# Kernel tuning notes

Hardware: AMD Instinct MI355X
Metric: run time of the kernel (lower is better)

## Reference

```python
import jax, jax.numpy as jnp
import numpy as np

NH, NOPE, ROPE, VD, KVL = 16, 128, 64, 128, 512
QHD = NOPE + ROPE  # 192
EPS = 1e-6
THETA = 10000.0


def rmsnorm(x, w):
    v = jnp.mean(x.astype(jnp.float32) ** 2, axis=-1, keepdims=True)
    return w * (x * jax.lax.rsqrt(v + EPS)).astype(x.dtype)


def _interleave_perm(x):
    # x.view(..., d//2, 2).transpose(-1, -2).reshape(..., d): [x0,x2,...,x1,x3,...]
    return jnp.concatenate([x[..., 0::2], x[..., 1::2]], axis=-1)


def _rotate_half(x):
    d = x.shape[-1] // 2
    return jnp.concatenate([-x[..., d:], x[..., :d]], axis=-1)


def _rope(x, cos, sin):
    x = _interleave_perm(x)
    return x * cos + _rotate_half(x) * sin


def reference(hidden_states, position_ids, q_a_w, q_a_ln, q_b_w, kv_a_w, kv_a_ln, kv_b_w, o_w):
    B, S, _ = hidden_states.shape
    h = hidden_states

    # low-rank Q: q_b(rmsnorm(q_a(h)))
    q = rmsnorm(h @ q_a_w.T, q_a_ln) @ q_b_w.T          # [B,S,NH*192]
    q = q.reshape(B, S, NH, QHD).transpose(0, 2, 1, 3)   # [B,NH,S,192]
    q_nope, q_pe = q[..., :NOPE], q[..., NOPE:]

    # compressed KV + shared rope key
    ckv = h @ kv_a_w.T                                    # [B,S,KVL+ROPE]
    compressed, k_pe = ckv[..., :KVL], ckv[..., KVL:]
    k_pe = k_pe.reshape(B, S, 1, ROPE).transpose(0, 2, 1, 3)  # [B,1,S,ROPE]

    kv = rmsnorm(compressed, kv_a_ln) @ kv_b_w.T          # [B,S,NH*(NOPE+VD)]
    kv = kv.reshape(B, S, NH, NOPE + VD).transpose(0, 2, 1, 3)
    k_nope, v = kv[..., :NOPE], kv[..., NOPE:]            # [B,NH,S,*]

    # rotary cache
    inv_freq = 1.0 / (THETA ** (jnp.arange(0, ROPE, 2, dtype=jnp.float32) / ROPE))
    t = jnp.arange(S, dtype=jnp.float32)
    freqs = jnp.outer(t, inv_freq)
    emb = jnp.concatenate([freqs, freqs], axis=-1)        # [S,ROPE]
    cos = jnp.cos(emb)[position_ids][:, None]             # [B,1,S,ROPE]
    sin = jnp.sin(emb)[position_ids][:, None]

    q_pe = _rope(q_pe, cos, sin)
    k_pe = _rope(k_pe, cos, sin)

    query = jnp.concatenate([q_nope, q_pe], axis=-1)                       # [B,NH,S,192]
    key = jnp.concatenate([k_nope, jnp.broadcast_to(k_pe, (B, NH, S, ROPE))], axis=-1)

    scale = QHD ** -0.5
    scores = jnp.einsum('bhqd,bhkd->bhqk', query, key) * scale
    causal = jnp.tril(jnp.ones((S, S), dtype=bool))
    scores = jnp.where(causal, scores, jnp.finfo(scores.dtype).min)
    attn = jax.nn.softmax(scores.astype(jnp.float32), axis=-1).astype(query.dtype)

    out = jnp.einsum('bhqk,bhkd->bhqd', attn, v)          # [B,NH,S,VD]
    out = out.transpose(0, 2, 1, 3).reshape(B, S, NH * VD)
    return out @ o_w.T


def setup_inputs():
    key = jax.random.key(0)
    ks = jax.random.split(key, 7)
    B, S, HID, QL = 2, 1024, 2048, 1536
    w = lambda i, shape: jax.random.normal(ks[i], shape, jnp.float32) / np.sqrt(shape[-1])
    return {
        'hidden_states': jax.random.normal(ks[0], (B, S, HID), jnp.float32),
        'position_ids': jnp.tile(jnp.arange(S, dtype=jnp.int32)[None, :], (B, 1)),
        'q_a_w': w(1, (QL, HID)),
        'q_a_ln': jnp.ones((QL,), jnp.float32),
        'q_b_w': w(2, (NH * QHD, QL)),
        'kv_a_w': w(3, (KVL + ROPE, HID)),
        'kv_a_ln': jnp.ones((KVL,), jnp.float32),
        'kv_b_w': w(4, (NH * (NOPE + VD), KVL)),
        'o_w': w(5, (HID, NH * VD)),
    }
```

## Files before the change

kernel.cpp:

```cpp
#include <hip/hip_runtime.h>
#include <stdint.h>
#include <math.h>

typedef unsigned short u16;
typedef __attribute__((ext_vector_type(8))) short short8;
typedef __attribute__((ext_vector_type(4))) short short4v;
typedef __attribute__((ext_vector_type(4))) float f32x4;

#define DEVFN static __device__ __forceinline__

DEVFN float bf2f(short b) {
  union { unsigned int i; float f; } u;
  u.i = ((unsigned int)(unsigned short)b) << 16;
  return u.f;
}
DEVFN short f2bf(float f) {
  union { float f; unsigned int i; } u; u.f = f;
  unsigned int r = u.i + 0x7fffu + ((u.i >> 16) & 1u);
  return (short)(r >> 16);
}

DEVFN f32x4 mfma32(short8 a, short8 b, f32x4 c) {
  return __builtin_amdgcn_mfma_f32_16x16x32_bf16(a, b, c, 0, 0, 0);
}
DEVFN f32x4 mfma16(short4v a, short4v b, f32x4 c) {
#if defined(__HIP_DEVICE_COMPILE__)
  return __builtin_amdgcn_mfma_f32_16x16x16bf16_1k(a, b, c, 0, 0, 0);
#else
  (void)a; (void)b; return c;
#endif
}

typedef const __attribute__((address_space(1))) unsigned int* gp_t;
typedef __attribute__((address_space(3))) unsigned int* lp_t;
typedef const __attribute__((address_space(3))) u16* lds_cp;
DEVFN void async_copy16(u16* lds, const u16* g) {
  __builtin_amdgcn_global_load_lds((gp_t)(const void*)g, (lp_t)(void*)lds, 16, 0, 0);
}
DEVFN short4v tr_read16(const u16* p) {
  short4v r;
  asm volatile("ds_read_b64_tr_b16 %0, %1" : "=v"(r) : "v"((lds_cp)(const void*)p));
  return r;
}
DEVFN void raw_barrier() {
  asm volatile("" ::: "memory");
  __builtin_amdgcn_s_barrier();
  asm volatile("" ::: "memory");
}

__global__ void cast_kernel(const float* __restrict__ in, u16* __restrict__ out, int n4) {
  int i = blockIdx.x * blockDim.x + threadIdx.x;
  if (i < n4) {
    f32x4 v = ((const f32x4*)in)[i];
    short4v o;
    o[0] = f2bf(v[0]); o[1] = f2bf(v[1]); o[2] = f2bf(v[2]); o[3] = f2bf(v[3]);
    ((short4v*)out)[i] = o;
  }
}

__global__ void rmsnorm_kernel(const u16* __restrict__ in, int istride,
                               u16* __restrict__ out, int ostride,
                               const float* __restrict__ w, int len) {
  const int row = blockIdx.x, t = threadIdx.x;
  short8 v = *(const short8*)(in + (size_t)row * istride + t * 8);
  float f[8]; float ss = 0.f;
#pragma unroll
  for (int j = 0; j < 8; ++j) { f[j] = bf2f(v[j]); ss += f[j] * f[j]; }
#pragma unroll
  for (int off = 1; off < 64; off <<= 1) ss += __shfl_xor(ss, off);
  __shared__ float red[8];
  int nw = (int)blockDim.x >> 6;
  if ((t & 63) == 0) red[t >> 6] = ss;
  __syncthreads();
  ss = 0.f;
  for (int i = 0; i < nw; ++i) ss += red[i];
  float r = rsqrtf(ss / (float)len + 1e-6f);
  const float* wp = w + t * 8;
  short8 ov;
#pragma unroll
  for (int j = 0; j < 8; ++j) ov[j] = f2bf(f[j] * r * wp[j]);
  *(short8*)(out + (size_t)row * ostride + t * 8) = ov;
}

__global__ void rope_kernel(const u16* __restrict__ q, const u16* __restrict__ ckv,
                            int cstride,
                            const int* __restrict__ pos_ids,
                            u16* __restrict__ qpe, u16* __restrict__ kpe) {
  const int row = blockIdx.x;
  const int t = threadIdx.x;
  const float pos = (float)pos_ids[row];
  const float L2TH = 13.287712379549449f;
  if (t < 32) {
    int i = t;
    float inv = exp2f(-L2TH * (float)i / 32.0f);
    float sv, cv; sincosf(pos * inv, &sv, &cv);
    float x0 = bf2f(ckv[(size_t)row * cstride + 512 + 2 * i]);
    float x1 = bf2f(ckv[(size_t)row * cstride + 512 + 2 * i + 1]);
    kpe[(size_t)row * 64 + i]      = (u16)f2bf(x0 * cv - x1 * sv);
    kpe[(size_t)row * 64 + 32 + i] = (u16)f2bf(x1 * cv + x0 * sv);
  }
#pragma unroll
  for (int j = 0; j < 8; ++j) {
    int idx = t + 64 * j;
    int hh = idx >> 5, i = idx & 31;
    float inv = exp2f(-L2TH * (float)i / 32.0f);
    float sv, cv; sincosf(pos * inv, &sv, &cv);
    const u16* base = q + (size_t)row * 3072 + hh * 192 + 128;
    float x0 = bf2f(base[2 * i]), x1 = bf2f(base[2 * i + 1]);
    u16* ob = qpe + ((size_t)row * 16 + hh) * 64;
    ob[i]      = (u16)f2bf(x0 * cv - x1 * sv);
    ob[32 + i] = (u16)f2bf(x1 * cv + x0 * sv);
  }
}

template <int BM, int BN, bool OUT_F32, int TAG>
__global__ __launch_bounds__(256) void gemm_bt(const u16* __restrict__ A,
                                               const u16* __restrict__ B,
                                               void* __restrict__ C,
                                               int M, int N, int K, int ldc) {
  constexpr int ACH = BM / 32;
  constexpr int BCH = BN / 32;
  constexpr int MI  = BM / 32;
  constexpr int NI  = BN / 32;
  constexpr int LOADS = ACH + BCH;
  __shared__ u16 As[2][BM * 64];
  __shared__ u16 Bs[2][BN * 64];
  const int tid = threadIdx.x;
  const int w = tid >> 6, l = tid & 63;
  const int lq = l & 15, lg = l >> 4;
  const int wm = (w >> 1) * (BM / 2);
  const int wn = (w & 1) * (BN / 2);

  const int f = blockIdx.x + gridDim.x * blockIdx.y;
  const int nwg = gridDim.x * gridDim.y;
  const int swz = (f & 7) * (nwg >> 3) + (f >> 3);
  const int bx = swz % gridDim.x, by = swz / gridDim.x;
  const int m0 = by * BM, n0 = bx * BN;

  const u16* srcA[ACH]; int dstA[ACH];
#pragma unroll
  for (int i = 0; i < ACH; ++i) {
    int c = i * 256 + tid;
    int row = c >> 3, pc = c & 7;
    int lc = pc ^ (row & 7);
    srcA[i] = A + (size_t)(m0 + row) * K + lc * 8;
    dstA[i] = c * 8;
  }
  const u16* srcB[BCH]; int dstB[BCH];
#pragma unroll
  for (int i = 0; i < BCH; ++i) {
    int c = i * 256 + tid;
    int row = c >> 3, pc = c & 7;
    int lc = pc ^ (row & 7);
    srcB[i] = B + (size_t)(n0 + row) * K + lc * 8;
    dstB[i] = c * 8;
  }

  auto stage = [&](int buf) {
#pragma unroll
    for (int i = 0; i < ACH; ++i) {
      async_copy16(&As[buf][dstA[i]], srcA[i]);
      srcA[i] += 64;
    }
#pragma unroll
    for (int i = 0; i < BCH; ++i) {
      async_copy16(&Bs[buf][dstB[i]], srcB[i]);
      srcB[i] += 64;
    }
  };

  f32x4 acc[MI][NI];
#pragma unroll
  for (int i = 0; i < MI; ++i)
#pragma unroll
    for (int j = 0; j < NI; ++j) acc[i][j] = (f32x4){0.f, 0.f, 0.f, 0.f};

  const int nt = K >> 6;
  stage(0);
  if (nt > 1) stage(1);

  for (int t = 0; t < nt; ++t) {
    if (t + 1 < nt) {
      if constexpr (LOADS == 4)      asm volatile("s_waitcnt vmcnt(4)" ::: "memory");
      else if constexpr (LOADS == 6) asm volatile("s_waitcnt vmcnt(6)" ::: "memory");
      else                           asm volatile("s_waitcnt vmcnt(8)" ::: "memory");
    } else {
      asm volatile("s_waitcnt vmcnt(0)" ::: "memory");
    }
    raw_barrier();

    const int buf = t & 1;
#pragma unroll
    for (int ks = 0; ks < 2; ++ks) {
      short8 af[MI], bfr[NI];
#pragma unroll
      for (int mi = 0; mi < MI; ++mi) {
        int row = wm + mi * 16 + lq;
        int ch = ((ks << 2) | lg) ^ (row & 7);
        af[mi] = *(const short8*)&As[buf][row * 64 + ch * 8];
      }
#pragma unroll
      for (int ni = 0; ni < NI; ++ni) {
        int row = wn + ni * 16 + lq;
        int ch = ((ks << 2) | lg) ^ (row & 7);
        bfr[ni] = *(const short8*)&Bs[buf][row * 64 + ch * 8];
      }
#pragma unroll
      for (int mi = 0; mi < MI; ++mi)
#pragma unroll
        for (int ni = 0; ni < NI; ++ni)
          acc[mi][ni] = mfma32(af[mi], bfr[ni], acc[mi][ni]);
    }

    raw_barrier();
    if (t + 2 < nt) stage(buf);
  }

#pragma unroll
  for (int mi = 0; mi < MI; ++mi) {
#pragma unroll
    for (int ni = 0; ni < NI; ++ni) {
      int col = n0 + wn + ni * 16 + lq;
#pragma unroll
      for (int r = 0; r < 4; ++r) {
        int rowm = m0 + wm + mi * 16 + lg * 4 + r;
        if constexpr (OUT_F32)
          ((float*)C)[(size_t)rowm * ldc + col] = acc[mi][ni][r];
        else
          ((u16*)C)[(size_t)rowm * ldc + col] = (u16)f2bf(acc[mi][ni][r]);
      }
    }
  }
}

__global__ __launch_bounds__(512, 4) void attn_kernel(const u16* __restrict__ q,
                                                      const u16* __restrict__ qpe,
                                                      const u16* __restrict__ kv,
                                                      const u16* __restrict__ kpe,
                                                      u16* __restrict__ o) {
  __shared__ u16 Ks[2][2][32 * 192];
  __shared__ u16 Vs[2][2][32 * 128];
  const int S = 1024;
  const int tid = threadIdx.x;
  const int w = tid >> 6, l = tid & 63;
  const int team = w >> 2, wt = w & 3;
  const int lq = l & 15, lg = l >> 4;
  const int h = blockIdx.y, b = blockIdx.z;
  const int chunk = b ? (15 - (int)blockIdx.x) : (int)blockIdx.x;
  const int q0 = chunk * 64 + wt * 16;
  const int nkt = chunk + 1;
  const size_t qrow = (size_t)b * S + q0 + lq;

  short8 qf[6];
#pragma unroll
  for (int c = 0; c < 4; ++c)
    qf[c] = *(const short8*)(q + qrow * 3072 + h * 192 + c * 32 + lg * 8);
#pragma unroll
  for (int c = 0; c < 2; ++c)
    qf[4 + c] = *(const short8*)(qpe + (qrow * 16 + h) * 64 + c * 32 + lg * 8);

  const size_t gb = (size_t)b * S + 32 * team;
  const u16* srcK[3]; int strK[3];
#pragma unroll
  for (int j = 0; j < 3; ++j) {
    int n = wt * 192 + j * 64 + l;
    int row = (n * 2731) >> 16;
    int pc = n - row * 24;
    int lc = (pc & ~7) | ((pc & 7) ^ (row & 7));
    if (lc < 16) { srcK[j] = kv + (gb + row) * 4096 + h * 256 + lc * 8; strK[j] = 64 * 4096; }
    else         { srcK[j] = kpe + (gb + row) * 64 + (lc - 16) * 8;     strK[j] = 64 * 64; }
  }
  const u16* srcV[2];
#pragma unroll
  for (int j = 0; j < 2; ++j) {
    int n = wt * 128 + j * 64 + l;
    int dsub = n >> 6, m = n & 63;
    int ksub = m >> 3, r = (m >> 1) & 3, half = m & 1;
    srcV[j] = kv + (gb + ksub * 4 + r) * 4096 + h * 256 + 128 + dsub * 16 + half * 8;
  }

  auto stage = [&](int buf) {
#pragma unroll
    for (int j = 0; j < 3; ++j) {
      async_copy16(&Ks[buf][team][(wt * 192 + j * 64) * 8], srcK[j]);
      srcK[j] += strK[j];
    }
#pragma unroll
    for (int j = 0; j < 2; ++j) {
      async_copy16(&Vs[buf][team][(wt * 128 + j * 64) * 8], srcV[j]);
      srcV[j] += 64 * 4096;
    }
  };

  const float scl = 0.07216878364870323f * 1.4426950408889634f;
  float m2 = -INFINITY, lsum = 0.f;
  f32x4 oac[8];
#pragma unroll
  for (int dt = 0; dt < 8; ++dt) oac[dt] = (f32x4){0.f, 0.f, 0.f, 0.f};

  const int e0 = (lg ^ (lq & 7)) << 4;
  const int vbase = lg * 64 + lq * 4;

  stage(0);
  asm volatile("s_waitcnt vmcnt(0)" ::: "memory");
  __syncthreads();

  int buf = 0;
  for (int i = 0; i < nkt; ++i) {
    if (i + 1 < nkt) stage(buf ^ 1);
    const int kbase = (2 * i + team) * 32;

    if (kbase <= q0 + 15) {
      const char* kb = (const char*)&Ks[buf][team][0];
      f32x4 sac0, sac1;
#pragma unroll
      for (int kt2 = 0; kt2 < 2; ++kt2) {
        int a0 = (kt2 * 16 + lq) * 384 + e0;
        int a1 = a0 ^ 64;
        f32x4 s = (f32x4){0.f, 0.f, 0.f, 0.f};
        s = mfma32(*(const short8*)(kb + a0),       qf[0], s);
        s = mfma32(*(const short8*)(kb + a1),       qf[1], s);
        s = mfma32(*(const short8*)(kb + a0 + 128), qf[2], s);
        s = mfma32(*(const short8*)(kb + a1 + 128), qf[3], s);
        s = mfma32(*(const short8*)(kb + a0 + 256), qf[4], s);
        s = mfma32(*(const short8*)(kb + a1 + 256), qf[5], s);
        if (kt2 == 0) sac0 = s; else sac1 = s;
      }

      const int qi = q0 + lq;
      const int kb0 = kbase + lg * 4;
      float s2[8];
#pragma unroll
      for (int r = 0; r < 4; ++r) {
        s2[r]     = (kb0 + r      <= qi) ? sac0[r] * scl : -INFINITY;
        s2[4 + r] = (kb0 + 16 + r <= qi) ? sac1[r] * scl : -INFINITY;
      }
      float mt = fmaxf(fmaxf(fmaxf(s2[0], s2[1]), fmaxf(s2[2], s2[3])),
                       fmaxf(fmaxf(s2[4], s2[5]), fmaxf(s2[6], s2[7])));
      mt = fmaxf(mt, __shfl_xor(mt, 16));
      mt = fmaxf(mt, __shfl_xor(mt, 32));
      float mnew = fmaxf(m2, mt);
      float resc = exp2f(m2 - mnew);
      float psum = 0.f;
#pragma unroll
      for (int r = 0; r < 8; ++r) { s2[r] = exp2f(s2[r] - mnew); psum += s2[r]; }
      psum += __shfl_xor(psum, 16);
      psum += __shfl_xor(psum, 32);
      lsum = lsum * resc + psum;
      m2 = mnew;
      short4v pf0, pf1;
#pragma unroll
      for (int r = 0; r < 4; ++r) { pf0[r] = f2bf(s2[r]); pf1[r] = f2bf(s2[4 + r]); }

#pragma unroll
      for (int hf = 0; hf < 2; ++hf) {
        short4v vf[4][2];
#pragma unroll
        for (int dd = 0; dd < 4; ++dd)
#pragma unroll
          for (int kt2 = 0; kt2 < 2; ++kt2)
            vf[dd][kt2] = tr_read16(&Vs[buf][team][vbase + (hf * 4 + dd) * 512 + kt2 * 256]);
        asm volatile("s_waitcnt lgkmcnt(0)" ::: "memory");
        __builtin_amdgcn_sched_barrier(0);
#pragma unroll
        for (int dd = 0; dd < 4; ++dd) {
          const int dt = hf * 4 + dd;
          f32x4 t = oac[dt];
          t[0] *= resc; t[1] *= resc; t[2] *= resc; t[3] *= resc;
          t = mfma16(vf[dd][0], pf0, t);
          t = mfma16(vf[dd][1], pf1, t);
          oac[dt] = t;
        }
      }
    }

    asm volatile("s_waitcnt vmcnt(0)" ::: "memory");
    __syncthreads();
    buf ^= 1;
  }

  float* MO = (float*)&Ks[0][0][0];
  float* MS = (float*)&Vs[0][0][0];
  const int qr = wt * 16 + lq;
  if (team == 1) {
#pragma unroll
    for (int dt = 0; dt < 8; ++dt)
#pragma unroll
      for (int r = 0; r < 4; ++r)
        MO[qr * 129 + dt * 16 + lg * 4 + r] = oac[dt][r];
    if (lg == 0) { MS[qr * 2] = m2; MS[qr * 2 + 1] = lsum; }
  }
  __syncthreads();
  if (team == 0) {
    float m1 = MS[qr * 2], l1 = MS[qr * 2 + 1];
    float mn = fmaxf(m2, m1);
    float a0 = exp2f(m2 - mn), a1 = exp2f(m1 - mn);
    float inv = 1.f / (lsum * a0 + l1 * a1);
#pragma unroll
    for (int dt = 0; dt < 8; ++dt)
#pragma unroll
      for (int r = 0; r < 4; ++r) {
        float val = (oac[dt][r] * a0 + MO[qr * 129 + dt * 16 + lg * 4 + r] * a1) * inv;
        o[((size_t)b * S + q0 + lq) * 2048 + h * 128 + dt * 16 + lg * 4 + r] = (u16)f2bf(val);
      }
  }
}

extern "C" void kernel_launch(void* const* d_in, const int* in_sizes, int n_in,
                              void* d_out, int out_size, void* d_ws, size_t ws_size,
                              hipStream_t stream) {
  const float* h_in  = (const float*)d_in[0];
  const int*   pos   = (const int*)d_in[1];
  const float* qaw   = (const float*)d_in[2];
  const float* qaln  = (const float*)d_in[3];
  const float* qbw   = (const float*)d_in[4];
  const float* kvaw  = (const float*)d_in[5];
  const float* kvaln = (const float*)d_in[6];
  const float* kvbw  = (const float*)d_in[7];
  const float* ow    = (const float*)d_in[8];
  float* out = (float*)d_out;

  const int M = 2048;
  char* p = (char*)d_ws;
  auto alloc = [&](size_t bytes) {
    char* r = p;
    p += (bytes + 255) & ~(size_t)255;
    return (u16*)r;
  };
  u16* h_bf = alloc((size_t)M * 2048 * 2);
  u16* W    = alloc((size_t)3072 * 1536 * 2);
  u16* F    = alloc((size_t)M * 2112 * 2);
  u16* qa   = alloc((size_t)M * 1536 * 2);
  u16* ckvn = alloc((size_t)M * 512 * 2);
  u16* qbuf = alloc((size_t)M * 3072 * 2);
  u16* kvb  = alloc((size_t)M * 4096 * 2);
  u16* qpe  = alloc((size_t)M * 16 * 64 * 2);
  u16* kpe  = alloc((size_t)M * 64 * 2);
  u16* attno = h_bf;

  dim3 blk(256);

  cast_kernel<<<4096, blk, 0, stream>>>(h_in, h_bf, 1048576);
  cast_kernel<<<3072, blk, 0, stream>>>(qaw, W, 786432);
  cast_kernel<<<1152, blk, 0, stream>>>(kvaw, W + (size_t)1536 * 2048, 294912);

  gemm_bt<128, 64, false, 1><<<dim3(33, 16), blk, 0, stream>>>(h_bf, W, F, M, 2112, 2048, 2112);
  rmsnorm_kernel<<<2048, 192, 0, stream>>>(F, 2112, qa, 1536, qaln, 1536);
  rmsnorm_kernel<<<2048, 64, 0, stream>>>(F + 1536, 2112, ckvn, 512, kvaln, 512);

  cast_kernel<<<4608, blk, 0, stream>>>(qbw, W, 1179648);
  gemm_bt<128, 64, false, 2><<<dim3(48, 16), blk, 0, stream>>>(qa, W, qbuf, M, 3072, 1536, 3072);

  cast_kernel<<<2048, blk, 0, stream>>>(kvbw, W, 524288);
  gemm_bt<128, 128, false, 4><<<dim3(32, 16), blk, 0, stream>>>(ckvn, W, kvb, M, 4096, 512, 4096);

  rope_kernel<<<2048, 64, 0, stream>>>(qbuf, F + 1536, 2112, pos, qpe, kpe);

  attn_kernel<<<dim3(16, 16, 2), 512, 0, stream>>>(qbuf, qpe, kvb, kpe, attno);

  cast_kernel<<<4096, blk, 0, stream>>>(ow, W, 1048576);
  gemm_bt<128, 64, true, 5><<<dim3(32, 16), blk, 0, stream>>>(attno, W, out, M, 2048, 2048, 2048);
}
```

Measured before the change: 176.2 us.

## Fuse input/weight casts into one launch and retile q_b GEMM to 128x96

```diff
diff --git a/kernel.cpp b/kernel.cpp
--- a/kernel.cpp
+++ b/kernel.cpp
@@ -56,6 +56,26 @@
     o[0] = f2bf(v[0]); o[1] = f2bf(v[1]); o[2] = f2bf(v[2]); o[3] = f2bf(v[3]);
     ((short4v*)out)[i] = o;
   }
+}
+
+__global__ void cast5_kernel(const float* __restrict__ s0, const float* __restrict__ s1,
+                             const float* __restrict__ s2, const float* __restrict__ s3,
+                             const float* __restrict__ s4,
+                             u16* __restrict__ d0, u16* __restrict__ d1,
+                             u16* __restrict__ d2, u16* __restrict__ d3,
+                             u16* __restrict__ d4) {
+  int i = blockIdx.x * blockDim.x + threadIdx.x;
+  const float* s; u16* d; int off;
+  if (i < 1048576)      { s = s0; d = d0; off = 0; }
+  else if (i < 1835008) { s = s1; d = d1; off = 1048576; }
+  else if (i < 2129920) { s = s2; d = d2; off = 1835008; }
+  else if (i < 3309568) { s = s3; d = d3; off = 2129920; }
+  else                  { s = s4; d = d4; off = 3309568; }
+  int j = i - off;
+  f32x4 v = ((const f32x4*)s)[j];
+  short4v o;
+  o[0] = f2bf(v[0]); o[1] = f2bf(v[1]); o[2] = f2bf(v[2]); o[3] = f2bf(v[3]);
+  ((short4v*)d)[j] = o;
 }
 
 __global__ void rmsnorm_kernel(const u16* __restrict__ in, int istride,
@@ -183,6 +203,7 @@
     if (t + 1 < nt) {
       if constexpr (LOADS == 4)      asm volatile("s_waitcnt vmcnt(4)" ::: "memory");
       else if constexpr (LOADS == 6) asm volatile("s_waitcnt vmcnt(6)" ::: "memory");
+      else if constexpr (LOADS == 7) asm volatile("s_waitcnt vmcnt(7)" ::: "memory");
       else                           asm volatile("s_waitcnt vmcnt(8)" ::: "memory");
     } else {
       asm volatile("s_waitcnt vmcnt(0)" ::: "memory");
@@ -427,37 +448,38 @@
     p += (bytes + 255) & ~(size_t)255;
     return (u16*)r;
   };
-  u16* h_bf = alloc((size_t)M * 2048 * 2);
-  u16* W    = alloc((size_t)3072 * 1536 * 2);
-  u16* F    = alloc((size_t)M * 2112 * 2);
-  u16* qa   = alloc((size_t)M * 1536 * 2);
-  u16* ckvn = alloc((size_t)M * 512 * 2);
-  u16* qbuf = alloc((size_t)M * 3072 * 2);
-  u16* kvb  = alloc((size_t)M * 4096 * 2);
-  u16* qpe  = alloc((size_t)M * 16 * 64 * 2);
-  u16* kpe  = alloc((size_t)M * 64 * 2);
+  u16* h_bf   = alloc((size_t)M * 2048 * 2);
+  u16* Wfused = alloc((size_t)2112 * 2048 * 2);
+  u16* Wqb    = alloc((size_t)3072 * 1536 * 2);
+  u16* Wkvb   = alloc((size_t)4096 * 512 * 2);
+  u16* F      = alloc((size_t)M * 2112 * 2);
+  u16* qbuf   = alloc((size_t)M * 3072 * 2);
+  u16* kvb    = alloc((size_t)M * 4096 * 2);
+  u16* qpe    = alloc((size_t)M * 16 * 64 * 2);
+  u16* kpe    = alloc((size_t)M * 64 * 2);
+  u16* qa    = Wfused;
+  u16* ckvn  = Wfused + (size_t)1536 * 2048;
   u16* attno = h_bf;
+  u16* OW    = qbuf;
 
   dim3 blk(256);
 
-  cast_kernel<<<4096, blk, 0, stream>>>(h_in, h_bf, 1048576);
-  cast_kernel<<<3072, blk, 0, stream>>>(qaw, W, 786432);
-  cast_kernel<<<1152, blk, 0, stream>>>(kvaw, W + (size_t)1536 * 2048, 294912);
-
-  gemm_bt<128, 64, false, 1><<<dim3(33, 16), blk, 0, stream>>>(h_bf, W, F, M, 2112, 2048, 2112);
+  cast5_kernel<<<14976, blk, 0, stream>>>(h_in, qaw, kvaw, qbw, kvbw,
+                                          h_bf, Wfused, Wfused + (size_t)1536 * 2048,
+                                          Wqb, Wkvb);
+
+  gemm_bt<128, 64, false, 1><<<dim3(33, 16), blk, 0, stream>>>(h_bf, Wfused, F, M, 2112, 2048, 2112);
   rmsnorm_kernel<<<2048, 192, 0, stream>>>(F, 2112, qa, 1536, qaln, 1536);
   rmsnorm_kernel<<<2048, 64, 0, stream>>>(F + 1536, 2112, ckvn, 512, kvaln, 512);
 
-  cast_kernel<<<4608, blk, 0, stream>>>(qbw, W, 1179648);
-  gemm_bt<128, 64, false, 2><<<dim3(48, 16), blk, 0, stream>>>(qa, W, qbuf, M, 3072, 1536, 3072);
-
-  cast_kernel<<<2048, blk, 0, stream>>>(kvbw, W, 524288);
-  gemm_bt<128, 128, false, 4><<<dim3(32, 16), blk, 0, stream>>>(ckvn, W, kvb, M, 4096, 512, 4096);
+  gemm_bt<128, 96, false, 2><<<dim3(32, 16), blk, 0, stream>>>(qa, Wqb, qbuf, M, 3072, 1536, 3072);
+
+  gemm_bt<128, 128, false, 4><<<dim3(32, 16), blk, 0, stream>>>(ckvn, Wkvb, kvb, M, 4096, 512, 4096);
 
   rope_kernel<<<2048, 64, 0, stream>>>(qbuf, F + 1536, 2112, pos, qpe, kpe);
 
   attn_kernel<<<dim3(16, 16, 2), 512, 0, stream>>>(qbuf, qpe, kvb, kpe, attno);
 
-  cast_kernel<<<4096, blk, 0, stream>>>(ow, W, 1048576);
-  gemm_bt<128, 64, true, 5><<<dim3(32, 16), blk, 0, stream>>>(attno, W, out, M, 2048, 2048, 2048);
-}
+  cast_kernel<<<4096, blk, 0, stream>>>(ow, OW, 1048576);
+  gemm_bt<128, 64, true, 5><<<dim3(32, 16), blk, 0, stream>>>(attno, OW, out, M, 2048, 2048, 2048);
+}
```

Measured after the change: 171.1 us. 2.9% less time.
